# Optimization experiments

Measured on AMD Instinct MI355X. Metric: run time of the kernel, lower is better.

## Reference

```python
import jax, jax.numpy as jnp
import numpy as np

N_NODES = 100000
N_EDGES = 1600000
IN_C, HID_C, OUT_C = 256, 128, 256


def setup_inputs() -> dict:
    key = jax.random.key(0)
    ks = jax.random.split(key, 8)
    x = jax.random.normal(ks[0], (N_NODES, IN_C), dtype=jnp.float32)
    src = jax.random.randint(ks[1], (N_EDGES,), 0, N_NODES, dtype=jnp.int64)
    dst = jnp.sort(jax.random.randint(ks[2], (N_EDGES,), 0, N_NODES, dtype=jnp.int64))
    # GraphConv weight [in, hid] (glorot), bias [hid]
    W_conv = jax.random.normal(ks[3], (IN_C, HID_C), dtype=jnp.float32) * (2.0 / (IN_C + HID_C)) ** 0.5
    b_conv = jnp.zeros((HID_C,), dtype=jnp.float32)
    # torch Linear weights are [out, in]
    W1 = jax.random.normal(ks[4], (HID_C, HID_C), dtype=jnp.float32) * (2.0 / (2 * HID_C)) ** 0.5
    b1 = jax.random.uniform(ks[5], (HID_C,), dtype=jnp.float32, minval=-1.0, maxval=1.0) / np.sqrt(HID_C)
    W2 = jax.random.normal(ks[6], (OUT_C, HID_C), dtype=jnp.float32) * (2.0 / (HID_C + OUT_C)) ** 0.5
    b2 = jax.random.uniform(ks[7], (OUT_C,), dtype=jnp.float32, minval=-1.0, maxval=1.0) / np.sqrt(OUT_C)
    return {"x": x, "src": src, "dst": dst, "W_conv": W_conv, "b_conv": b_conv,
            "W1": W1, "b1": b1, "W2": W2, "b2": b2}


def reference(x, src, dst, W_conv, b_conv, W1, b1, W2, b2):
    N = x.shape[0]
    ones = jnp.ones(src.shape[0], dtype=x.dtype)
    out_deg = jnp.clip(jax.ops.segment_sum(ones, src, num_segments=N), 1.0)  # [N]
    in_deg = jnp.clip(jax.ops.segment_sum(ones, dst, num_segments=N), 1.0)   # [N]
    # DGL GraphConv, norm='both', in_feats > out_feats -> weight applied before aggregation
    h = x * jax.lax.rsqrt(out_deg)[:, None]          # src-side normalization
    h = h @ W_conv                                    # [N, hid]
    m = jax.ops.segment_sum(h[src], dst, num_segments=N, indices_are_sorted=True)
    h = m * jax.lax.rsqrt(in_deg)[:, None] + b_conv   # dst-side normalization + bias
    h = jax.nn.relu(h)
    h = jax.nn.relu(h @ W1.T + b1)
    return h @ W2.T + b2
```

## Files before the change

### kernel.cpp

```cpp
#include <hip/hip_runtime.h>
#include <hip/hip_bf16.h>


typedef __attribute__((ext_vector_type(8))) short short8;
typedef __attribute__((ext_vector_type(4))) float f32x4;

static __device__ __forceinline__ float bf2f(unsigned int u16) {
    union { unsigned int i; float f; } c; c.i = u16 << 16; return c.f;
}
static __device__ __forceinline__ ushort f2bf(float f) {
    union { float f; unsigned int i; } c; c.f = f;
    unsigned int i = c.i;
    return (ushort)((i + 0x7FFFu + ((i >> 16) & 1u)) >> 16);
}

constexpr int NCHUNK   = 256;
constexpr int NBUK_MAX = 512;
constexpr int WPREP_BLOCKS = (128 * 256 + 128 * 128 + 256 * 128) / 256;

__global__ __launch_bounds__(256) void prep_kernel(
    const float* __restrict__ Wc, const float* __restrict__ W1,
    const float* __restrict__ W2, ushort* __restrict__ WcT,
    ushort* __restrict__ W1b, ushort* __restrict__ W2b,
    const int* __restrict__ src, int* __restrict__ M,
    const int* __restrict__ dst, int* __restrict__ row_ptr,
    int nE, int N, int nBuk, int chunkSz)
{
    __shared__ int cnt[NBUK_MAX];
    const int bid = blockIdx.x, tid = threadIdx.x;

    if (bid < WPREP_BLOCKS) {
        int i = bid * 256 + tid;
        if (i < 128 * 256) {
            int o = i >> 8, k = i & 255;
            WcT[o * 256 + k] = f2bf(Wc[k * 128 + o]);
        } else if (i < 128 * 256 + 128 * 128) {
            int j = i - 128 * 256;
            W1b[j] = f2bf(W1[j]);
        } else {
            int j = i - 128 * 256 - 128 * 128;
            W2b[j] = f2bf(W2[j]);
        }
        return;
    }
    if (bid < WPREP_BLOCKS + NCHUNK) {
        int c = bid - WPREP_BLOCKS;
        for (int i = tid; i < nBuk; i += 256) cnt[i] = 0;
        __syncthreads();
        int e0 = c * chunkSz, e1 = min(e0 + chunkSz, nE);
        for (int e = e0 + tid; e < e1; e += 256)
            atomicAdd(&cnt[src[e] >> 8], 1);
        __syncthreads();
        for (int b = tid; b < nBuk; b += 256)
            M[b * NCHUNK + c] = cnt[b];
        return;
    }
    int e = (bid - WPREP_BLOCKS - NCHUNK) * 256 + tid;
    if (e >= nE) return;
    int d = dst[e];
    if (e == 0) {
        for (int n = 0; n <= d; ++n) row_ptr[n] = 0;
    } else {
        int p = dst[e - 1];
        for (int n = p + 1; n <= d; ++n) row_ptr[n] = e;
    }
    if (e == nE - 1) {
        for (int n = d + 1; n <= N; ++n) row_ptr[n] = nE;
    }
}

__global__ __launch_bounds__(256) void scanA_kernel(
    int* __restrict__ M, int* __restrict__ tot)
{
    __shared__ int buf[2][NCHUNK];
    int b = blockIdx.x, tid = threadIdx.x;
    int v = M[b * NCHUNK + tid];
    buf[0][tid] = v;
    __syncthreads();
    int pi = 0;
#pragma unroll
    for (int off = 1; off < NCHUNK; off <<= 1) {
        int t = buf[pi][tid];
        if (tid >= off) t += buf[pi][tid - off];
        buf[pi ^ 1][tid] = t;
        __syncthreads();
        pi ^= 1;
    }
    int incl = buf[pi][tid];
    M[b * NCHUNK + tid] = incl - v;
    if (tid == NCHUNK - 1) tot[b] = incl;
}

static __device__ __forceinline__ void scan_bb(
    const int* __restrict__ tot, int* bb_l, int nBuk, int tid)
{
    if (tid < 64) {
        int base = 0;
        for (int i0 = 0; i0 < nBuk; i0 += 64) {
            int i = i0 + tid;
            int v = (i < nBuk) ? tot[i] : 0;
            int orig = v;
#pragma unroll
            for (int off = 1; off < 64; off <<= 1) {
                int u = __shfl_up(v, off, 64);
                if (tid >= off) v += u;
            }
            if (i < nBuk) bb_l[i] = base + v - orig;
            base += __shfl(v, 63, 64);
        }
        if (tid == 0) bb_l[nBuk] = base;
    }
    __syncthreads();
}

__global__ __launch_bounds__(256) void scatter_keys_kernel(
    const int* __restrict__ src, const int* __restrict__ M,
    const int* __restrict__ tot, int* __restrict__ ss,
    int nE, int nBuk, int chunkSz)
{
    __shared__ int cur[NBUK_MAX];
    __shared__ int bb_l[NBUK_MAX + 1];
    int c = blockIdx.x, tid = threadIdx.x;
    scan_bb(tot, bb_l, nBuk, tid);
    for (int i = tid; i < nBuk; i += 256)
        cur[i] = M[i * NCHUNK + c] + bb_l[i];
    __syncthreads();
    int e0 = c * chunkSz, e1 = min(e0 + chunkSz, nE);
    for (int e = e0 + tid; e < e1; e += 256) {
        int s = src[e];
        int pos = atomicAdd(&cur[s >> 8], 1);
        ss[pos] = s;
    }
}

__global__ __launch_bounds__(256) void count_kernel(
    const int* __restrict__ ss, const int* __restrict__ tot,
    int* __restrict__ outdeg, int N, int nBuk)
{
    __shared__ int hist[256];
    __shared__ int bb_l[NBUK_MAX + 1];
    int b = blockIdx.x, tid = threadIdx.x;
    hist[tid] = 0;
    scan_bb(tot, bb_l, nBuk, tid);
    int e0 = bb_l[b], e1 = bb_l[b + 1];
    for (int e = e0 + tid; e < e1; e += 256)
        atomicAdd(&hist[ss[e] & 255], 1);
    __syncthreads();
    int n = b * 256 + tid;
    if (n < N) outdeg[n] = hist[tid];
}

__global__ __launch_bounds__(512, 4) void gemm1_kernel(
    const float* __restrict__ A, const ushort* __restrict__ B,
    const int* __restrict__ outdeg, ushort* __restrict__ C, int nRows)
{
    __shared__ ushort Bs[128 * 256];
    __shared__ ushort As[128 * 64];
    __shared__ float rowscale[128];

    const int tid  = threadIdx.x;
    const int lane = tid & 63;
    const int w    = tid >> 6;
    const int wm   = w >> 1;
    const int wn   = w & 1;
    const int r    = lane & 15;
    const int q    = lane >> 4;
    const int row0 = blockIdx.x * 128;

    if (tid < 128) {
        int g = row0 + tid;
        int dv = (g < nRows) ? outdeg[g] : 1;
        rowscale[tid] = rsqrtf((float)max(dv, 1));
    }

#pragma unroll
    for (int s = 0; s < 8; ++s) {
        int idx = s * 512 + tid;
        int col = idx >> 5, kg = idx & 31;
        *(short8*)&Bs[col * 256 + ((kg ^ (col & 7)) * 8)] =
            *(const short8*)&B[(size_t)col * 256 + kg * 8];
    }

    int arow0 = tid >> 3,          akg0 = tid & 7;
    int arow1 = (512 + tid) >> 3,  akg1 = (512 + tid) & 7;

    float4 areg[2][2][2];

#define G1_ISSUE(cc, bb)                                                     \
    {                                                                        \
        int g0 = row0 + arow0, g1 = row0 + arow1;                            \
        areg[bb][0][0] = make_float4(0.f, 0.f, 0.f, 0.f);                    \
        areg[bb][0][1] = make_float4(0.f, 0.f, 0.f, 0.f);                    \
        areg[bb][1][0] = make_float4(0.f, 0.f, 0.f, 0.f);                    \
        areg[bb][1][1] = make_float4(0.f, 0.f, 0.f, 0.f);                    \
        if (g0 < nRows) {                                                    \
            const float* p = &A[(size_t)g0 * 256 + (cc) * 64 + akg0 * 8];    \
            areg[bb][0][0] = *(const float4*)p;                              \
            areg[bb][0][1] = *(const float4*)(p + 4);                        \
        }                                                                    \
        if (g1 < nRows) {                                                    \
            const float* p = &A[(size_t)g1 * 256 + (cc) * 64 + akg1 * 8];    \
            areg[bb][1][0] = *(const float4*)p;                              \
            areg[bb][1][1] = *(const float4*)(p + 4);                        \
        }                                                                    \
    }

    G1_ISSUE(0, 0)
    G1_ISSUE(1, 1)

    f32x4 acc[8];
#pragma unroll
    for (int t = 0; t < 8; ++t) acc[t] = (f32x4){0.f, 0.f, 0.f, 0.f};

#pragma unroll
    for (int c = 0; c < 4; ++c) {
        if (c > 0) __syncthreads();
        const int buf = c & 1;
#pragma unroll
        for (int s = 0; s < 2; ++s) {
            int arow = s ? arow1 : arow0;
            int akg  = s ? akg1  : akg0;
            float4 v0 = areg[buf][s][0], v1 = areg[buf][s][1];
            ushort u[8];
            u[0] = f2bf(v0.x); u[1] = f2bf(v0.y); u[2] = f2bf(v0.z); u[3] = f2bf(v0.w);
            u[4] = f2bf(v1.x); u[5] = f2bf(v1.y); u[6] = f2bf(v1.z); u[7] = f2bf(v1.w);
            *(short8*)&As[arow * 64 + ((akg ^ (arow & 7)) * 8)] = *(const short8*)u;
        }
        if (c + 2 < 4) G1_ISSUE(c + 2, buf)
        __syncthreads();
#pragma unroll
        for (int ks = 0; ks < 2; ++ks) {
            int sA = ks * 4 + q;
            int ra0 = wm * 32 + r, ra1 = wm * 32 + 16 + r;
            short8 a0 = *(const short8*)&As[ra0 * 64 + ((sA ^ (ra0 & 7)) * 8)];
            short8 a1 = *(const short8*)&As[ra1 * 64 + ((sA ^ (ra1 & 7)) * 8)];
            int sB = c * 8 + ks * 4 + q;
#pragma unroll
            for (int t = 0; t < 4; ++t) {
                int col = wn * 64 + t * 16 + r;
                short8 b = *(const short8*)&Bs[col * 256 + ((sB ^ (col & 7)) * 8)];
                acc[t]     = __builtin_amdgcn_mfma_f32_16x16x32_bf16(a0, b, acc[t], 0, 0, 0);
                acc[4 + t] = __builtin_amdgcn_mfma_f32_16x16x32_bf16(a1, b, acc[4 + t], 0, 0, 0);
            }
        }
    }
#undef G1_ISSUE

#pragma unroll
    for (int fr = 0; fr < 2; ++fr)
#pragma unroll
        for (int t = 0; t < 4; ++t) {
            int col = wn * 64 + t * 16 + r;
#pragma unroll
            for (int reg = 0; reg < 4; ++reg) {
                int lr = wm * 32 + fr * 16 + q * 4 + reg;
                int g = row0 + lr;
                if (g < nRows)
                    C[(size_t)g * 128 + col] = f2bf(acc[fr * 4 + t][reg] * rowscale[lr]);
            }
        }
}

__global__ __launch_bounds__(256) void gather_kernel(
    const ushort* __restrict__ h1, const int* __restrict__ src,
    const int* __restrict__ rp, const float* __restrict__ b_conv,
    ushort* __restrict__ h2, int N)
{
    int n = (blockIdx.x * 256 + threadIdx.x) >> 6;
    int lane = threadIdx.x & 63;
    if (n >= N) return;
    const int g = lane >> 4;
    const int c = lane & 15;
    int e0 = rp[n], e1 = rp[n + 1];

    float a[8];
#pragma unroll
    for (int j = 0; j < 8; ++j) a[j] = 0.f;

    int e = e0 + g;
    for (; e + 12 < e1; e += 16) {
        int s0 = src[e], s1 = src[e + 4], s2 = src[e + 8], s3 = src[e + 12];
        short8 v0 = *(const short8*)&h1[((size_t)(unsigned)s0 << 7) + c * 8];
        short8 v1 = *(const short8*)&h1[((size_t)(unsigned)s1 << 7) + c * 8];
        short8 v2 = *(const short8*)&h1[((size_t)(unsigned)s2 << 7) + c * 8];
        short8 v3 = *(const short8*)&h1[((size_t)(unsigned)s3 << 7) + c * 8];
#pragma unroll
        for (int j = 0; j < 8; ++j)
            a[j] += (bf2f((unsigned short)v0[j]) + bf2f((unsigned short)v1[j]))
                  + (bf2f((unsigned short)v2[j]) + bf2f((unsigned short)v3[j]));
    }
    for (; e < e1; e += 4) {
        short8 v0 = *(const short8*)&h1[((size_t)(unsigned)src[e] << 7) + c * 8];
#pragma unroll
        for (int j = 0; j < 8; ++j)
            a[j] += bf2f((unsigned short)v0[j]);
    }

#pragma unroll
    for (int j = 0; j < 8; ++j) {
        a[j] += __shfl_xor(a[j], 16, 64);
        a[j] += __shfl_xor(a[j], 32, 64);
    }

    if (g == 0) {
        float sc = rsqrtf((float)max(e1 - e0, 1));
        ushort o[8];
#pragma unroll
        for (int j = 0; j < 8; ++j)
            o[j] = f2bf(fmaxf(fmaf(a[j], sc, b_conv[c * 8 + j]), 0.f));
        *(short8*)&h2[((size_t)(unsigned)n << 7) + c * 8] = *(const short8*)o;
    }
}

__global__ __launch_bounds__(512) void gemm23_kernel(
    const ushort* __restrict__ A, const ushort* __restrict__ W1b,
    const ushort* __restrict__ W2b, const float* __restrict__ b1,
    const float* __restrict__ b2, float* __restrict__ out, int nRows)
{
    __shared__ ushort AsTs[128 * 128];
    __shared__ ushort Ws[128 * 128];

    const int tid  = threadIdx.x;
    const int lane = tid & 63;
    const int w    = tid >> 6;
    const int wm   = w >> 1;
    const int wn   = w & 1;
    const int r    = lane & 15;
    const int q    = lane >> 4;
    const int row0 = blockIdx.x * 128;

#pragma unroll
    for (int s = 0; s < 4; ++s) {
        int idx = s * 512 + tid;
        int row = idx >> 4, kg = idx & 15;
        int g = row0 + row;
        short8 v = (short8){0, 0, 0, 0, 0, 0, 0, 0};
        if (g < nRows) v = *(const short8*)&A[(size_t)g * 128 + kg * 8];
        *(short8*)&AsTs[row * 128 + ((kg ^ (row & 7)) * 8)] = v;
    }
#pragma unroll
    for (int s = 0; s < 4; ++s) {
        int idx = s * 512 + tid;
        int col = idx >> 4, kg = idx & 15;
        *(short8*)&Ws[col * 128 + ((kg ^ (col & 7)) * 8)] =
            *(const short8*)&W1b[(size_t)col * 128 + kg * 8];
    }
    __syncthreads();

    f32x4 acc1[8];
#pragma unroll
    for (int t = 0; t < 8; ++t) acc1[t] = (f32x4){0.f, 0.f, 0.f, 0.f};
#pragma unroll
    for (int ks = 0; ks < 4; ++ks) {
        int sA = ks * 4 + q;
        int ra0 = wm * 32 + r, ra1 = wm * 32 + 16 + r;
        short8 a0 = *(const short8*)&AsTs[ra0 * 128 + ((sA ^ (ra0 & 7)) * 8)];
        short8 a1 = *(const short8*)&AsTs[ra1 * 128 + ((sA ^ (ra1 & 7)) * 8)];
#pragma unroll
        for (int t = 0; t < 4; ++t) {
            int col = wn * 64 + t * 16 + r;
            short8 b = *(const short8*)&Ws[col * 128 + ((sA ^ (col & 7)) * 8)];
            acc1[t]     = __builtin_amdgcn_mfma_f32_16x16x32_bf16(a0, b, acc1[t], 0, 0, 0);
            acc1[4 + t] = __builtin_amdgcn_mfma_f32_16x16x32_bf16(a1, b, acc1[4 + t], 0, 0, 0);
        }
    }
    __syncthreads();

#pragma unroll
    for (int fr = 0; fr < 2; ++fr)
#pragma unroll
        for (int t = 0; t < 4; ++t) {
            int col = wn * 64 + t * 16 + r;
            float bo = b1[col];
#pragma unroll
            for (int reg = 0; reg < 4; ++reg) {
                int row = wm * 32 + fr * 16 + q * 4 + reg;
                float v = fmaxf(acc1[fr * 4 + t][reg] + bo, 0.f);
                AsTs[row * 128 + (((col >> 3) ^ (row & 7)) * 8) + (col & 7)] = f2bf(v);
            }
        }
#pragma unroll
    for (int s = 0; s < 4; ++s) {
        int idx = s * 512 + tid;
        int col = idx >> 4, kg = idx & 15;
        *(short8*)&Ws[col * 128 + ((kg ^ (col & 7)) * 8)] =
            *(const short8*)&W2b[(size_t)col * 128 + kg * 8];
    }
    __syncthreads();

    f32x4 acc2[16];
#pragma unroll
    for (int t = 0; t < 16; ++t) acc2[t] = (f32x4){0.f, 0.f, 0.f, 0.f};
#pragma unroll
    for (int ks = 0; ks < 4; ++ks) {
        int sA = ks * 4 + q;
        int ra0 = wm * 32 + r, ra1 = wm * 32 + 16 + r;
        short8 a0 = *(const short8*)&AsTs[ra0 * 128 + ((sA ^ (ra0 & 7)) * 8)];
        short8 a1 = *(const short8*)&AsTs[ra1 * 128 + ((sA ^ (ra1 & 7)) * 8)];
#pragma unroll
        for (int t = 0; t < 4; ++t) {
            int col = wn * 64 + t * 16 + r;
            short8 b = *(const short8*)&Ws[col * 128 + ((sA ^ (col & 7)) * 8)];
            acc2[t]     = __builtin_amdgcn_mfma_f32_16x16x32_bf16(a0, b, acc2[t], 0, 0, 0);
            acc2[4 + t] = __builtin_amdgcn_mfma_f32_16x16x32_bf16(a1, b, acc2[4 + t], 0, 0, 0);
        }
    }
    __syncthreads();

#pragma unroll
    for (int s = 0; s < 4; ++s) {
        int idx = s * 512 + tid;
        int col = idx >> 4, kg = idx & 15;
        *(short8*)&Ws[col * 128 + ((kg ^ (col & 7)) * 8)] =
            *(const short8*)&W2b[(size_t)(128 + col) * 128 + kg * 8];
    }
    __syncthreads();

#pragma unroll
    for (int ks = 0; ks < 4; ++ks) {
        int sA = ks * 4 + q;
        int ra0 = wm * 32 + r, ra1 = wm * 32 + 16 + r;
        short8 a0 = *(const short8*)&AsTs[ra0 * 128 + ((sA ^ (ra0 & 7)) * 8)];
        short8 a1 = *(const short8*)&AsTs[ra1 * 128 + ((sA ^ (ra1 & 7)) * 8)];
#pragma unroll
        for (int t = 0; t < 4; ++t) {
            int col = wn * 64 + t * 16 + r;
            short8 b = *(const short8*)&Ws[col * 128 + ((sA ^ (col & 7)) * 8)];
            acc2[8 + t]  = __builtin_amdgcn_mfma_f32_16x16x32_bf16(a0, b, acc2[8 + t], 0, 0, 0);
            acc2[12 + t] = __builtin_amdgcn_mfma_f32_16x16x32_bf16(a1, b, acc2[12 + t], 0, 0, 0);
        }
    }

#pragma unroll
    for (int h = 0; h < 2; ++h)
#pragma unroll
        for (int fr = 0; fr < 2; ++fr)
#pragma unroll
            for (int t = 0; t < 4; ++t) {
                int col = h * 128 + wn * 64 + t * 16 + r;
                float bo = b2[col];
#pragma unroll
                for (int reg = 0; reg < 4; ++reg) {
                    int g = row0 + wm * 32 + fr * 16 + q * 4 + reg;
                    if (g < nRows)
                        out[(size_t)g * 256 + col] = acc2[h * 8 + fr * 4 + t][reg] + bo;
                }
            }
}

extern "C" void kernel_launch(void* const* d_in, const int* in_sizes, int n_in,
                              void* d_out, int out_size, void* d_ws, size_t ws_size,
                              hipStream_t stream)
{
    const float* x      = (const float*)d_in[0];
    const int*   src    = (const int*)d_in[1];
    const int*   dst    = (const int*)d_in[2];
    const float* W_conv = (const float*)d_in[3];
    const float* b_conv = (const float*)d_in[4];
    const float* W1     = (const float*)d_in[5];
    const float* b1     = (const float*)d_in[6];
    const float* W2     = (const float*)d_in[7];
    const float* b2     = (const float*)d_in[8];
    float* out = (float*)d_out;

    const int N  = in_sizes[0] / 256;
    const int nE = in_sizes[1];

    const int nBuk    = (N + 255) >> 8;
    const int chunkSz = (nE + NCHUNK - 1) / NCHUNK;

    ushort* h1  = (ushort*)d_ws;
    ushort* h2  = h1 + (size_t)N * 128;
    ushort* WcT = h2 + (size_t)N * 128;
    ushort* W1b = WcT + 128 * 256;
    ushort* W2b = W1b + 128 * 128;
    int* outdeg = (int*)(W2b + 256 * 128);
    int* rp     = outdeg + N;
    int* tot    = rp + (N + 1);
    int* M      = tot + nBuk;
    int* ss     = M + nBuk * NCHUNK;

    const int rowptrBlocks = (nE + 255) / 256;
    prep_kernel<<<WPREP_BLOCKS + NCHUNK + rowptrBlocks, 256, 0, stream>>>(
        W_conv, W1, W2, WcT, W1b, W2b, src, M, dst, rp, nE, N, nBuk, chunkSz);

    scanA_kernel<<<nBuk, 256, 0, stream>>>(M, tot);
    scatter_keys_kernel<<<NCHUNK, 256, 0, stream>>>(src, M, tot, ss, nE, nBuk, chunkSz);
    count_kernel<<<nBuk, 256, 0, stream>>>(ss, tot, outdeg, N, nBuk);

    const int nBlocks128 = (N + 127) / 128;
    gemm1_kernel<<<nBlocks128, 512, 0, stream>>>(x, WcT, outdeg, h1, N);

    gather_kernel<<<(N * 64 + 255) / 256, 256, 0, stream>>>(
        h1, src, rp, b_conv, h2, N);

    gemm23_kernel<<<nBlocks128, 512, 0, stream>>>(h2, W1b, W2b, b1, b2, out, N);
}
```

Baseline: 174.6 us.

## Fuse out-degree counting into gemm1 and deepen its A-tile pipeline

Removes the separate count_kernel. Each gemm1 block now sums bucket totals to find its src bucket range and builds a shared-memory histogram of out-degrees for its 128 rows, computed while the A loads are in flight. The A tile K-chunk shrinks from 64 to 32, with triple buffering over 8 iterations and a new swizzle. The gather kernel's bf16 unpack now uses shift and mask on uint4 loads. This drops one launch and the outdeg round trip through global memory, but each pair of gemm blocks rescans the same 256-node bucket and the k-loop now has more barriers.

```diff
diff --git a/kernel.cpp b/kernel.cpp
--- a/kernel.cpp
+++ b/kernel.cpp
@@ -133,30 +133,15 @@
     }
 }
 
-__global__ __launch_bounds__(256) void count_kernel(
-    const int* __restrict__ ss, const int* __restrict__ tot,
-    int* __restrict__ outdeg, int N, int nBuk)
-{
-    __shared__ int hist[256];
-    __shared__ int bb_l[NBUK_MAX + 1];
-    int b = blockIdx.x, tid = threadIdx.x;
-    hist[tid] = 0;
-    scan_bb(tot, bb_l, nBuk, tid);
-    int e0 = bb_l[b], e1 = bb_l[b + 1];
-    for (int e = e0 + tid; e < e1; e += 256)
-        atomicAdd(&hist[ss[e] & 255], 1);
-    __syncthreads();
-    int n = b * 256 + tid;
-    if (n < N) outdeg[n] = hist[tid];
-}
-
 __global__ __launch_bounds__(512, 4) void gemm1_kernel(
     const float* __restrict__ A, const ushort* __restrict__ B,
-    const int* __restrict__ outdeg, ushort* __restrict__ C, int nRows)
+    const int* __restrict__ ss, const int* __restrict__ tot,
+    ushort* __restrict__ C, int nRows, int nBuk)
 {
     __shared__ ushort Bs[128 * 256];
-    __shared__ ushort As[128 * 64];
-    __shared__ float rowscale[128];
+    __shared__ ushort As[128 * 32];
+    __shared__ int hist[128];
+    __shared__ int eRange[2];
 
     const int tid  = threadIdx.x;
     const int lane = tid & 63;
@@ -167,12 +152,6 @@
     const int q    = lane >> 4;
     const int row0 = blockIdx.x * 128;
 
-    if (tid < 128) {
-        int g = row0 + tid;
-        int dv = (g < nRows) ? outdeg[g] : 1;
-        rowscale[tid] = rsqrtf((float)max(dv, 1));
-    }
-
 #pragma unroll
     for (int s = 0; s < 8; ++s) {
         int idx = s * 512 + tid;
@@ -180,61 +159,74 @@
         *(short8*)&Bs[col * 256 + ((kg ^ (col & 7)) * 8)] =
             *(const short8*)&B[(size_t)col * 256 + kg * 8];
     }
-
-    int arow0 = tid >> 3,          akg0 = tid & 7;
-    int arow1 = (512 + tid) >> 3,  akg1 = (512 + tid) & 7;
-
-    float4 areg[2][2][2];
+    if (tid < 128) hist[tid] = 0;
+
+    if (w == 0) {
+        int bk = blockIdx.x >> 1;
+        int partial = 0;
+        for (int i = lane; i < bk; i += 64) partial += tot[i];
+#pragma unroll
+        for (int off = 32; off >= 1; off >>= 1)
+            partial += __shfl_xor(partial, off, 64);
+        if (lane == 0) {
+            eRange[0] = partial;
+            eRange[1] = partial + tot[bk];
+        }
+    }
+
+    const int arow = tid >> 2, akg = tid & 3;
+    const int aslot = (akg ^ ((arow >> 1) & 3)) * 8;
+
+    float4 areg[3][2];
 
 #define G1_ISSUE(cc, bb)                                                     \
     {                                                                        \
-        int g0 = row0 + arow0, g1 = row0 + arow1;                            \
-        areg[bb][0][0] = make_float4(0.f, 0.f, 0.f, 0.f);                    \
-        areg[bb][0][1] = make_float4(0.f, 0.f, 0.f, 0.f);                    \
-        areg[bb][1][0] = make_float4(0.f, 0.f, 0.f, 0.f);                    \
-        areg[bb][1][1] = make_float4(0.f, 0.f, 0.f, 0.f);                    \
+        int g0 = row0 + arow;                                                \
+        areg[bb][0] = make_float4(0.f, 0.f, 0.f, 0.f);                       \
+        areg[bb][1] = make_float4(0.f, 0.f, 0.f, 0.f);                       \
         if (g0 < nRows) {                                                    \
-            const float* p = &A[(size_t)g0 * 256 + (cc) * 64 + akg0 * 8];    \
-            areg[bb][0][0] = *(const float4*)p;                              \
-            areg[bb][0][1] = *(const float4*)(p + 4);                        \
-        }                                                                    \
-        if (g1 < nRows) {                                                    \
-            const float* p = &A[(size_t)g1 * 256 + (cc) * 64 + akg1 * 8];    \
-            areg[bb][1][0] = *(const float4*)p;                              \
-            areg[bb][1][1] = *(const float4*)(p + 4);                        \
+            const float* p = &A[(size_t)g0 * 256 + (cc) * 32 + akg * 8];     \
+            areg[bb][0] = *(const float4*)p;                                 \
+            areg[bb][1] = *(const float4*)(p + 4);                           \
         }                                                                    \
     }
 
     G1_ISSUE(0, 0)
     G1_ISSUE(1, 1)
+    G1_ISSUE(2, 2)
+    __syncthreads();
+
+    {
+        int e0 = eRange[0], e1 = eRange[1];
+        for (int e = e0 + tid; e < e1; e += 512) {
+            int s = ss[e];
+            if ((s >> 7) == blockIdx.x)
+                atomicAdd(&hist[s & 127], 1);
+        }
+    }
 
     f32x4 acc[8];
 #pragma unroll
     for (int t = 0; t < 8; ++t) acc[t] = (f32x4){0.f, 0.f, 0.f, 0.f};
 
 #pragma unroll
-    for (int c = 0; c < 4; ++c) {
+    for (int c = 0; c < 8; ++c) {
         if (c > 0) __syncthreads();
-        const int buf = c & 1;
-#pragma unroll
-        for (int s = 0; s < 2; ++s) {
-            int arow = s ? arow1 : arow0;
-            int akg  = s ? akg1  : akg0;
-            float4 v0 = areg[buf][s][0], v1 = areg[buf][s][1];
+        const int buf = c % 3;
+        {
+            float4 v0 = areg[buf][0], v1 = areg[buf][1];
             ushort u[8];
             u[0] = f2bf(v0.x); u[1] = f2bf(v0.y); u[2] = f2bf(v0.z); u[3] = f2bf(v0.w);
             u[4] = f2bf(v1.x); u[5] = f2bf(v1.y); u[6] = f2bf(v1.z); u[7] = f2bf(v1.w);
-            *(short8*)&As[arow * 64 + ((akg ^ (arow & 7)) * 8)] = *(const short8*)u;
-        }
-        if (c + 2 < 4) G1_ISSUE(c + 2, buf)
+            *(short8*)&As[arow * 32 + aslot] = *(const short8*)u;
+        }
+        if (c + 3 < 8) G1_ISSUE(c + 3, buf)
         __syncthreads();
-#pragma unroll
-        for (int ks = 0; ks < 2; ++ks) {
-            int sA = ks * 4 + q;
+        {
             int ra0 = wm * 32 + r, ra1 = wm * 32 + 16 + r;
-            short8 a0 = *(const short8*)&As[ra0 * 64 + ((sA ^ (ra0 & 7)) * 8)];
-            short8 a1 = *(const short8*)&As[ra1 * 64 + ((sA ^ (ra1 & 7)) * 8)];
-            int sB = c * 8 + ks * 4 + q;
+            short8 a0 = *(const short8*)&As[ra0 * 32 + ((q ^ ((ra0 >> 1) & 3)) * 8)];
+            short8 a1 = *(const short8*)&As[ra1 * 32 + ((q ^ ((ra1 >> 1) & 3)) * 8)];
+            int sB = c * 4 + q;
 #pragma unroll
             for (int t = 0; t < 4; ++t) {
                 int col = wn * 64 + t * 16 + r;
@@ -255,10 +247,24 @@
             for (int reg = 0; reg < 4; ++reg) {
                 int lr = wm * 32 + fr * 16 + q * 4 + reg;
                 int g = row0 + lr;
-                if (g < nRows)
-                    C[(size_t)g * 128 + col] = f2bf(acc[fr * 4 + t][reg] * rowscale[lr]);
+                if (g < nRows) {
+                    float sc = rsqrtf((float)max(hist[lr], 1));
+                    C[(size_t)g * 128 + col] = f2bf(acc[fr * 4 + t][reg] * sc);
+                }
             }
         }
+}
+
+static __device__ __forceinline__ void acc8(float* a, uint4 u) {
+    union { unsigned int i; float f; } c;
+    c.i = u.x << 16;          a[0] += c.f;
+    c.i = u.x & 0xffff0000u;  a[1] += c.f;
+    c.i = u.y << 16;          a[2] += c.f;
+    c.i = u.y & 0xffff0000u;  a[3] += c.f;
+    c.i = u.z << 16;          a[4] += c.f;
+    c.i = u.z & 0xffff0000u;  a[5] += c.f;
+    c.i = u.w << 16;          a[6] += c.f;
+    c.i = u.w & 0xffff0000u;  a[7] += c.f;
 }
 
 __global__ __launch_bounds__(256) void gather_kernel(
@@ -280,20 +286,15 @@
     int e = e0 + g;
     for (; e + 12 < e1; e += 16) {
         int s0 = src[e], s1 = src[e + 4], s2 = src[e + 8], s3 = src[e + 12];
-        short8 v0 = *(const short8*)&h1[((size_t)(unsigned)s0 << 7) + c * 8];
-        short8 v1 = *(const short8*)&h1[((size_t)(unsigned)s1 << 7) + c * 8];
-        short8 v2 = *(const short8*)&h1[((size_t)(unsigned)s2 << 7) + c * 8];
-        short8 v3 = *(const short8*)&h1[((size_t)(unsigned)s3 << 7) + c * 8];
-#pragma unroll
-        for (int j = 0; j < 8; ++j)
-            a[j] += (bf2f((unsigned short)v0[j]) + bf2f((unsigned short)v1[j]))
-                  + (bf2f((unsigned short)v2[j]) + bf2f((unsigned short)v3[j]));
+        uint4 u0 = *(const uint4*)&h1[((size_t)(unsigned)s0 << 7) + c * 8];
+        uint4 u1 = *(const uint4*)&h1[((size_t)(unsigned)s1 << 7) + c * 8];
+        uint4 u2 = *(const uint4*)&h1[((size_t)(unsigned)s2 << 7) + c * 8];
+        uint4 u3 = *(const uint4*)&h1[((size_t)(unsigned)s3 << 7) + c * 8];
+        acc8(a, u0); acc8(a, u1); acc8(a, u2); acc8(a, u3);
     }
     for (; e < e1; e += 4) {
-        short8 v0 = *(const short8*)&h1[((size_t)(unsigned)src[e] << 7) + c * 8];
-#pragma unroll
-        for (int j = 0; j < 8; ++j)
-            a[j] += bf2f((unsigned short)v0[j]);
+        uint4 u0 = *(const uint4*)&h1[((size_t)(unsigned)src[e] << 7) + c * 8];
+        acc8(a, u0);
     }
 
 #pragma unroll
@@ -474,8 +475,7 @@
     ushort* WcT = h2 + (size_t)N * 128;
     ushort* W1b = WcT + 128 * 256;
     ushort* W2b = W1b + 128 * 128;
-    int* outdeg = (int*)(W2b + 256 * 128);
-    int* rp     = outdeg + N;
+    int* rp     = (int*)(W2b + 256 * 128);
     int* tot    = rp + (N + 1);
     int* M      = tot + nBuk;
     int* ss     = M + nBuk * NCHUNK;
@@ -486,10 +486,9 @@
 
     scanA_kernel<<<nBuk, 256, 0, stream>>>(M, tot);
     scatter_keys_kernel<<<NCHUNK, 256, 0, stream>>>(src, M, tot, ss, nE, nBuk, chunkSz);
-    count_kernel<<<nBuk, 256, 0, stream>>>(ss, tot, outdeg, N, nBuk);
 
     const int nBlocks128 = (N + 127) / 128;
-    gemm1_kernel<<<nBlocks128, 512, 0, stream>>>(x, WcT, outdeg, h1, N);
+    gemm1_kernel<<<nBlocks128, 512, 0, stream>>>(x, WcT, ss, tot, h1, N, nBuk);
 
     gather_kernel<<<(N * 64 + 255) / 256, 256, 0, stream>>>(
         h1, src, rp, b_conv, h2, N);
```

Result: faster. 164.0 us (-6.1%).
